# Kernel tuning notes

Hardware: AMD Instinct MI355X
Metric: run time of the kernel (lower is better)

## Reference

```python
import jax, jax.numpy as jnp
import numpy as np
import math

B, S, IN_DIM = 4, 2048, 512
D, H, L, FF = 256, 4, 4, 2048
HD = D // H
EPS = 1e-5


def _pos_encoding(S, D, dtype=jnp.float32):
    pos = jnp.arange(S, dtype=jnp.float32)[:, None]
    div = jnp.exp(jnp.arange(0, D, 2, dtype=jnp.float32) * (-math.log(10000.0) / D))
    pe = jnp.zeros((S, D), dtype=jnp.float32)
    pe = pe.at[:, 0::2].set(jnp.sin(pos * div))
    pe = pe.at[:, 1::2].set(jnp.cos(pos * div))
    return pe.astype(dtype)


def _layernorm(x, w, b):
    mu = jnp.mean(x, axis=-1, keepdims=True)
    var = jnp.var(x, axis=-1, keepdims=True)
    return (x - mu) * jax.lax.rsqrt(var + EPS) * w + b


def setup_inputs() -> dict:
    key = jax.random.key(0)
    ks = jax.random.split(key, 12)
    sc = 0.02
    inp = {
        "x": jax.random.normal(ks[0], (B, S, IN_DIM), dtype=jnp.float32),
        "W_in": jax.random.normal(ks[1], (D, IN_DIM), dtype=jnp.float32) * sc,
        "b_in": jnp.zeros((D,), dtype=jnp.float32),
        "qkv_w": jax.random.normal(ks[2], (L, 3 * D, D), dtype=jnp.float32) * sc,
        "qkv_b": jnp.zeros((L, 3 * D), dtype=jnp.float32),
        "out_w": jax.random.normal(ks[3], (L, D, D), dtype=jnp.float32) * sc,
        "out_b": jnp.zeros((L, D), dtype=jnp.float32),
        "ln1_w": jnp.ones((L, D), dtype=jnp.float32),
        "ln1_b": jnp.zeros((L, D), dtype=jnp.float32),
        "ff1_w": jax.random.normal(ks[4], (L, FF, D), dtype=jnp.float32) * sc,
        "ff1_b": jnp.zeros((L, FF), dtype=jnp.float32),
        "ff2_w": jax.random.normal(ks[5], (L, D, FF), dtype=jnp.float32) * sc,
        "ff2_b": jnp.zeros((L, D), dtype=jnp.float32),
        "ln2_w": jnp.ones((L, D), dtype=jnp.float32),
        "ln2_b": jnp.zeros((L, D), dtype=jnp.float32),
        "W_fc": jax.random.normal(ks[6], (IN_DIM, D), dtype=jnp.float32) * sc,
        "b_fc": jnp.zeros((IN_DIM,), dtype=jnp.float32),
    }
    return inp


def reference(x, W_in, b_in, qkv_w, qkv_b, out_w, out_b, ln1_w, ln1_b,
              ff1_w, ff1_b, ff2_w, ff2_b, ln2_w, ln2_b, W_fc, b_fc):
    # input projection + positional encoding (dropout=0 / eval)
    h = jnp.einsum('bsi,di->bsd', x, W_in) + b_in
    h = h + _pos_encoding(S, D, h.dtype)[None]

    scale = 1.0 / math.sqrt(HD)
    for l in range(L):
        # --- self-attention (unfused: explicit QK^T + softmax + V) ---
        qkv = jnp.einsum('bsd,ed->bse', h, qkv_w[l]) + qkv_b[l]  # [B,S,3D]
        q, k, v = jnp.split(qkv, 3, axis=-1)
        q = q.reshape(B, S, H, HD).transpose(0, 2, 1, 3)  # [B,H,S,HD]
        k = k.reshape(B, S, H, HD).transpose(0, 2, 1, 3)
        v = v.reshape(B, S, H, HD).transpose(0, 2, 1, 3)
        scores = jnp.einsum('bhqd,bhkd->bhqk', q, k) * scale  # [B,H,S,S]
        attn = jax.nn.softmax(scores, axis=-1)
        ctx = jnp.einsum('bhqk,bhkd->bhqd', attn, v)
        ctx = ctx.transpose(0, 2, 1, 3).reshape(B, S, D)
        sa = jnp.einsum('bsd,ed->bse', ctx, out_w[l]) + out_b[l]
        h = _layernorm(h + sa, ln1_w[l], ln1_b[l])  # post-norm
        # --- feed-forward (relu) ---
        ff = jax.nn.relu(jnp.einsum('bsd,fd->bsf', h, ff1_w[l]) + ff1_b[l])
        ff = jnp.einsum('bsf,df->bsd', ff, ff2_w[l]) + ff2_b[l]
        h = _layernorm(h + ff, ln2_w[l], ln2_b[l])

    # final projection from last time step
    return jnp.einsum('bd,od->bo', h[:, -1, :], W_fc) + b_fc  # [B, IN_DIM]
```

## Files before the change

kernel.cpp:

```cpp
#include <hip/hip_runtime.h>
#include <math.h>

#define S_LEN 2048
#define DMODEL 256
#define NHEAD 4
#define HDIM 64
#define NLAYER 4
#define FFDIM 2048
#define INDIM 512
#define BATCH 4
#define NTOK (BATCH * S_LEN)
#define EPSV 1e-5f
#define KSPLIT 4

typedef __attribute__((ext_vector_type(8))) short frag8;
typedef __attribute__((ext_vector_type(4))) float f32x4v;
typedef unsigned short u16;
typedef unsigned int u32;

__device__ __forceinline__ float pe_val(int s, int d) {
    const float c = 0.035977892f;
    float dv = expf(-(float)(d & ~1) * c);
    float arg = (float)s * dv;
    return (d & 1) ? cosf(arg) : sinf(arg);
}

__device__ __forceinline__ u16 f2bf(float f) {
    union { float f; unsigned u; } v; v.f = f;
    unsigned r = v.u + 0x7fffu + ((v.u >> 16) & 1u);
    return (u16)(r >> 16);
}
__device__ __forceinline__ float bf2f(u16 h) {
    union { u32 u; float f; } v; v.u = (u32)h << 16; return v.f;
}
__device__ __forceinline__ u32 pk2bf(float lo, float hi) {
    union { float f; u32 u; } a, b; a.f = lo; b.f = hi;
    return __builtin_amdgcn_perm(b.u, a.u, 0x07060302u);
}
__device__ __forceinline__ void load_lds16(const u16* g, u16* l) {
    __builtin_amdgcn_global_load_lds(
        (const __attribute__((address_space(1))) unsigned int*)g,
        (__attribute__((address_space(3))) unsigned int*)l, 16, 0, 0);
}

__global__ __launch_bounds__(256) void cvt_all(
    const float* __restrict__ x, const float* __restrict__ W_in,
    const float* __restrict__ qkv_w, const float* __restrict__ out_w,
    const float* __restrict__ ff1_w, const float* __restrict__ ff2_w,
    u16* __restrict__ xb, u16* __restrict__ W_in_b,
    u16* __restrict__ qkv_w_b, u16* __restrict__ out_w_b,
    u16* __restrict__ ff1_w_b, u16* __restrict__ ff2_w_b)
{
    const int i = blockIdx.x * 256 + threadIdx.x;
    const float* src; u16* dst; int base;
    if (i < 1048576)      { src = x;     dst = xb;      base = 0; }
    else if (i < 1081344) { src = W_in;  dst = W_in_b;  base = 1048576; }
    else if (i < 1277952) { src = qkv_w; dst = qkv_w_b; base = 1081344; }
    else if (i < 1343488) { src = out_w; dst = out_w_b; base = 1277952; }
    else if (i < 1867776) { src = ff1_w; dst = ff1_w_b; base = 1343488; }
    else                  { src = ff2_w; dst = ff2_w_b; base = 1867776; }
    const int e = (i - base) * 4;
    const float4 v = *(const float4*)(src + e);
    ushort4 o;
    o.x = f2bf(v.x); o.y = f2bf(v.y); o.z = f2bf(v.z); o.w = f2bf(v.w);
    *(ushort4*)(dst + e) = o;
}

template <int MODE>
__global__ __launch_bounds__(256) void gemm_mfma(
    const u16* __restrict__ A, const u16* __restrict__ W,
    const float* __restrict__ bias, u16* __restrict__ Cb,
    int M, int N, int K)
{
    __shared__ __align__(16) u16 As[128 * 32];
    __shared__ __align__(16) u16 Bs[128 * 32];
    const int t = threadIdx.x;
    const int w = t >> 6, lane = t & 63;
    const int col = lane & 15, quad = lane >> 4;
    const int qx = (quad ^ ((col >> 1) & 3)) * 8;
    const int m0 = blockIdx.x * 128, n0 = blockIdx.y * 128;
    const int wm = (w >> 1) * 64, wn = (w & 1) * 64;

    const int r0 = lane >> 2;
    const int kc = ((lane & 3) ^ ((lane >> 3) & 3)) * 8;
    const u16* pA0 = A + (size_t)(m0 + (w * 2 + 0) * 16 + r0) * K + kc;
    const u16* pA1 = A + (size_t)(m0 + (w * 2 + 1) * 16 + r0) * K + kc;
    const u16* pB0 = W + (size_t)(n0 + (w * 2 + 0) * 16 + r0) * K + kc;
    const u16* pB1 = W + (size_t)(n0 + (w * 2 + 1) * 16 + r0) * K + kc;
    u16* lA0 = As + (w * 2 + 0) * 512;
    u16* lA1 = As + (w * 2 + 1) * 512;
    u16* lB0 = Bs + (w * 2 + 0) * 512;
    u16* lB1 = Bs + (w * 2 + 1) * 512;

    f32x4v acc[4][4];
#pragma unroll
    for (int i = 0; i < 4; ++i)
#pragma unroll
        for (int j = 0; j < 4; ++j) acc[i][j] = (f32x4v){0.f, 0.f, 0.f, 0.f};

    for (int kb = 0; kb < K; kb += 32) {
        __syncthreads();
        load_lds16(pA0 + kb, lA0);
        load_lds16(pA1 + kb, lA1);
        load_lds16(pB0 + kb, lB0);
        load_lds16(pB1 + kb, lB1);
        __syncthreads();

        frag8 a[4], b[4];
#pragma unroll
        for (int i = 0; i < 4; ++i)
            a[i] = *(const frag8*)&As[(wm + i * 16 + col) * 32 + qx];
#pragma unroll
        for (int j = 0; j < 4; ++j)
            b[j] = *(const frag8*)&Bs[(wn + j * 16 + col) * 32 + qx];
#pragma unroll
        for (int i = 0; i < 4; ++i)
#pragma unroll
            for (int j = 0; j < 4; ++j)
                acc[i][j] = __builtin_amdgcn_mfma_f32_16x16x32_bf16(
                    a[i], b[j], acc[i][j], 0, 0, 0);
    }

#pragma unroll
    for (int j = 0; j < 4; ++j) {
        const int cn = n0 + wn + j * 16 + col;
        const float bv = bias[cn];
#pragma unroll
        for (int i = 0; i < 4; ++i) {
            const int cmb = m0 + wm + i * 16 + quad * 4;
#pragma unroll
            for (int r = 0; r < 4; ++r) {
                float v = acc[i][j][r] + bv;
                if (MODE == 2) v = fmaxf(v, 0.f);
                Cb[(size_t)(cmb + r) * N + cn] = f2bf(v);
            }
        }
    }
}

template <int MODE>
__global__ __launch_bounds__(256) void gemm64k(
    const u16* __restrict__ A, const u16* __restrict__ W,
    const float* __restrict__ bias, u16* __restrict__ Cb,
    u16* __restrict__ aux, const float* __restrict__ lp,
    int M, int N, int K)
{
    __shared__ __align__(16) u16 As[2][64 * 64];
    __shared__ __align__(16) u16 Bs[2][64 * 64];
    const int t = threadIdx.x;
    const int w = t >> 6, lane = t & 63;
    const int col = lane & 15, quad = lane >> 4;
    const int px0 = ((quad ^ (col & 7))) * 8;
    const int px1 = px0 ^ 32;
    const int m0 = blockIdx.x * 64, n0 = blockIdx.y * 64;
    const int wm = (w >> 1) * 32, wn = (w & 1) * 32;

    const int sr = lane >> 3;
    const int lc = ((lane & 7) ^ sr) * 8;
    const u16* pA0 = A + (size_t)(m0 + w * 16 + sr) * K + lc;
    const u16* pA1 = A + (size_t)(m0 + w * 16 + 8 + sr) * K + lc;
    const u16* pB0 = W + (size_t)(n0 + w * 16 + sr) * K + lc;
    const u16* pB1 = W + (size_t)(n0 + w * 16 + 8 + sr) * K + lc;
    const int o0 = (w * 16) * 64, o1 = (w * 16 + 8) * 64;

    f32x4v acc[2][2];
#pragma unroll
    for (int i = 0; i < 2; ++i)
#pragma unroll
        for (int j = 0; j < 2; ++j) acc[i][j] = (f32x4v){0.f, 0.f, 0.f, 0.f};

    auto stageA = [&](int it, int buf) {
        if (MODE == 6) {
            const int hh = it;
#pragma unroll
            for (int pos = 0; pos < 2; ++pos) {
                const int m = m0 + w * 16 + pos * 8 + sr;
                const int q = m & (S_LEN - 1);
                const int bh = (m >> 11) * 4 + hh;
                const size_t basei = (((size_t)bh) * S_LEN + q) * 64 + lc;
                float l = 0.f;
                float o[8] = {0.f, 0.f, 0.f, 0.f, 0.f, 0.f, 0.f, 0.f};
#pragma unroll
                for (int ksx = 0; ksx < KSPLIT; ++ksx) {
                    const uint4 pv = *(const uint4*)(A + (size_t)ksx * 16 * S_LEN * 64 + basei);
                    o[0] += bf2f((u16)(pv.x & 0xffff)); o[1] += bf2f((u16)(pv.x >> 16));
                    o[2] += bf2f((u16)(pv.y & 0xffff)); o[3] += bf2f((u16)(pv.y >> 16));
                    o[4] += bf2f((u16)(pv.z & 0xffff)); o[5] += bf2f((u16)(pv.z >> 16));
                    o[6] += bf2f((u16)(pv.w & 0xffff)); o[7] += bf2f((u16)(pv.w >> 16));
                    l += lp[((size_t)ksx * 16 + bh) * S_LEN + q];
                }
                const float inv = 1.f / l;
                uint4 pk;
                pk.x = ((u32)f2bf(o[1] * inv) << 16) | f2bf(o[0] * inv);
                pk.y = ((u32)f2bf(o[3] * inv) << 16) | f2bf(o[2] * inv);
                pk.z = ((u32)f2bf(o[5] * inv) << 16) | f2bf(o[4] * inv);
                pk.w = ((u32)f2bf(o[7] * inv) << 16) | f2bf(o[6] * inv);
                *(uint4*)&As[buf][(pos ? o1 : o0) + lane * 8] = pk;
            }
        } else {
            const int kb = it << 6;
            load_lds16(pA0 + kb, &As[buf][o0]);
            load_lds16(pA1 + kb, &As[buf][o1]);
        }
    };
    auto stageB = [&](int it, int buf) {
        const int kb = it << 6;
        load_lds16(pB0 + kb, &Bs[buf][o0]);
        load_lds16(pB1 + kb, &Bs[buf][o1]);
    };

    stageA(0, 0);
    stageB(0, 0);

    const int NIT = K >> 6;
    for (int it = 0; it < NIT; ++it) {
        const int cur = it & 1;
        __syncthreads();
        if (it + 1 < NIT) {
            stageA(it + 1, cur ^ 1);
            stageB(it + 1, cur ^ 1);
        }
#pragma unroll
        for (int kh = 0; kh < 2; ++kh) {
            const int px = kh ? px1 : px0;
            frag8 a[2], b[2];
#pragma unroll
            for (int i = 0; i < 2; ++i)
                a[i] = *(const frag8*)&As[cur][(wm + i * 16 + col) * 64 + px];
#pragma unroll
            for (int j = 0; j < 2; ++j)
                b[j] = *(const frag8*)&Bs[cur][(wn + j * 16 + col) * 64 + px];
#pragma unroll
            for (int i = 0; i < 2; ++i)
#pragma unroll
                for (int j = 0; j < 2; ++j)
                    acc[i][j] = __builtin_amdgcn_mfma_f32_16x16x32_bf16(
                        a[i], b[j], acc[i][j], 0, 0, 0);
        }
    }

#pragma unroll
    for (int j = 0; j < 2; ++j) {
        const int cn = n0 + wn + j * 16 + col;
        const float bv = bias[cn];
#pragma unroll
        for (int i = 0; i < 2; ++i) {
            const int cmb = m0 + wm + i * 16 + quad * 4;
            float vv[4];
#pragma unroll
            for (int r = 0; r < 4; ++r) {
                float v = acc[i][j][r] + bv;
                if (MODE == 1) v += pe_val((cmb + r) & (S_LEN - 1), cn);
                if (MODE == 5 || MODE == 6)
                    v += bf2f(aux[(size_t)(cmb + r) * N + cn]);
                vv[r] = v;
                Cb[(size_t)(cmb + r) * N + cn] = f2bf(v);
            }
            if (MODE == 4 && cn >= 512) {
                const int dg = cn - 512;
                const int bh = (cmb >> 11) * 4 + (dg >> 6);
                uint2 pk;
                pk.x = ((u32)f2bf(vv[1]) << 16) | f2bf(vv[0]);
                pk.y = ((u32)f2bf(vv[3]) << 16) | f2bf(vv[2]);
                *(uint2*)&aux[((size_t)bh * 64 + (dg & 63)) * S_LEN + (cmb & 2047)] = pk;
            }
        }
    }
}

__global__ __launch_bounds__(256) void attn_part(const u16* __restrict__ qkv,
                                                 const u16* __restrict__ vt,
                                                 u16* __restrict__ Opart,
                                                 float* __restrict__ lpart)
{
    __shared__ __align__(16) u16 Ks0[64 * 32], Ks1[64 * 32];
    __shared__ __align__(16) u16 Vt0[64 * 32], Vt1[64 * 32];
    __shared__ __align__(16) u16 Ps[4][2][2][512];

    const int t = threadIdx.x;
    const int w = t >> 6, lane = t & 63;
    const int col = lane & 15, quad = lane >> 4;
    const int sq = (col >> 1) & 3;
    const int qx = (quad ^ sq) * 8;
    const int bh = blockIdx.x, b = bh >> 2, hh = bh & 3;
    const int qt = blockIdx.y, ks = blockIdx.z;

    const float SCL = 0.125f * 1.44269504f;

    frag8 qf[2][2];
#pragma unroll
    for (int qg = 0; qg < 2; ++qg) {
        const int qrow = qt * 128 + w * 32 + qg * 16 + col;
        const u16* qp = qkv + (size_t)(b * S_LEN + qrow) * 768 + hh * HDIM;
        const frag8 r0 = *(const frag8*)(qp + quad * 8);
        const frag8 r1 = *(const frag8*)(qp + 32 + quad * 8);
#pragma unroll
        for (int e = 0; e < 8; ++e) {
            qf[qg][0][e] = (short)f2bf(bf2f((u16)r0[e]) * SCL);
            qf[qg][1][e] = (short)f2bf(bf2f((u16)r1[e]) * SCL);
        }
    }
    frag8 ones;
#pragma unroll
    for (int e = 0; e < 8; ++e) ones[e] = (short)0x3F80;

    f32x4v Oacc[2][4], lacc[2];
#pragma unroll
    for (int qg = 0; qg < 2; ++qg) {
#pragma unroll
        for (int dt = 0; dt < 4; ++dt) Oacc[qg][dt] = (f32x4v){0.f, 0.f, 0.f, 0.f};
        lacc[qg] = (f32x4v){0.f, 0.f, 0.f, 0.f};
    }

    const int srow = w * 16 + (lane >> 2);
    const int sseg = ((lane & 3) ^ ((lane >> 3) & 3)) * 8;
    const int kb0 = ks * (S_LEN / KSPLIT);
    const u16* kbase = qkv + (size_t)(b * S_LEN + kb0 + srow) * 768
                       + 256 + hh * HDIM + sseg;
    const u16* vbase = vt + ((size_t)bh * 64 + srow) * S_LEN + kb0 + sseg;
    u16* lK0 = Ks0 + w * 512;
    u16* lK1 = Ks1 + w * 512;
    u16* lV0 = Vt0 + w * 512;
    u16* lV1 = Vt1 + w * 512;

    for (int kt = 0; kt < S_LEN / KSPLIT / 64; ++kt) {
        __syncthreads();
        const u16* kp = kbase + (size_t)kt * 64 * 768;
        const u16* vp = vbase + kt * 64;
        load_lds16(kp, lK0);
        load_lds16(kp + 32, lK1);
        load_lds16(vp, lV0);
        load_lds16(vp + 32, lV1);
        __syncthreads();

#pragma unroll
        for (int nt = 0; nt < 4; ++nt) {
            const frag8 k0 = *(const frag8*)&Ks0[(nt * 16 + col) * 32 + qx];
            const frag8 k1 = *(const frag8*)&Ks1[(nt * 16 + col) * 32 + qx];
            const int c = (nt & 1) * 2 + (quad >> 1);
            const int poff = col * 32 + ((c ^ sq) * 8) + (quad & 1) * 4;
#pragma unroll
            for (int qg = 0; qg < 2; ++qg) {
                f32x4v s = (f32x4v){0.f, 0.f, 0.f, 0.f};
                s = __builtin_amdgcn_mfma_f32_16x16x32_bf16(k0, qf[qg][0], s, 0, 0, 0);
                s = __builtin_amdgcn_mfma_f32_16x16x32_bf16(k1, qf[qg][1], s, 0, 0, 0);
                const float p0 = __builtin_amdgcn_exp2f(s[0]);
                const float p1 = __builtin_amdgcn_exp2f(s[1]);
                const float p2 = __builtin_amdgcn_exp2f(s[2]);
                const float p3 = __builtin_amdgcn_exp2f(s[3]);
                uint2 pk;
                pk.x = pk2bf(p0, p1);
                pk.y = pk2bf(p2, p3);
                *(uint2*)&Ps[w][qg][nt >> 1][poff] = pk;
            }
        }

        frag8 pf[2][2];
#pragma unroll
        for (int qg = 0; qg < 2; ++qg) {
            pf[qg][0] = *(const frag8*)&Ps[w][qg][0][col * 32 + qx];
            pf[qg][1] = *(const frag8*)&Ps[w][qg][1][col * 32 + qx];
        }
#pragma unroll
        for (int dt = 0; dt < 4; ++dt) {
            const frag8 v0 = *(const frag8*)&Vt0[(dt * 16 + col) * 32 + qx];
            const frag8 v1 = *(const frag8*)&Vt1[(dt * 16 + col) * 32 + qx];
#pragma unroll
            for (int qg = 0; qg < 2; ++qg) {
                Oacc[qg][dt] = __builtin_amdgcn_mfma_f32_16x16x32_bf16(
                    v0, pf[qg][0], Oacc[qg][dt], 0, 0, 0);
                Oacc[qg][dt] = __builtin_amdgcn_mfma_f32_16x16x32_bf16(
                    v1, pf[qg][1], Oacc[qg][dt], 0, 0, 0);
            }
        }
#pragma unroll
        for (int qg = 0; qg < 2; ++qg) {
            lacc[qg] = __builtin_amdgcn_mfma_f32_16x16x32_bf16(
                ones, pf[qg][0], lacc[qg], 0, 0, 0);
            lacc[qg] = __builtin_amdgcn_mfma_f32_16x16x32_bf16(
                ones, pf[qg][1], lacc[qg], 0, 0, 0);
        }
    }

#pragma unroll
    for (int qg = 0; qg < 2; ++qg) {
        const int qrow = qt * 128 + w * 32 + qg * 16 + col;
        u16* op = Opart + (((size_t)ks * 16 + bh) * S_LEN + qrow) * 64;
#pragma unroll
        for (int dt = 0; dt < 4; ++dt) {
            uint2 pk;
            pk.x = pk2bf(Oacc[qg][dt][0], Oacc[qg][dt][1]);
            pk.y = pk2bf(Oacc[qg][dt][2], Oacc[qg][dt][3]);
            *(uint2*)(op + dt * 16 + quad * 4) = pk;
        }
        if (quad == 0)
            lpart[((size_t)ks * 16 + bh) * S_LEN + qrow] = lacc[qg][0];
    }
}

__global__ __launch_bounds__(256) void ln_only(u16* __restrict__ hb,
                                               const u16* __restrict__ sab,
                                               const float* __restrict__ w,
                                               const float* __restrict__ b)
{
    const int t = blockIdx.x;
    const int d = threadIdx.x;
    const size_t idx = (size_t)t * DMODEL + d;
    const float x = bf2f(sab[idx]);

    float s = x, s2 = x * x;
#pragma unroll
    for (int off = 32; off; off >>= 1) {
        s += __shfl_down(s, off);
        s2 += __shfl_down(s2, off);
    }
    __shared__ float ls[4], ls2[4];
    __shared__ float mu_s, rs_s;
    const int wid = d >> 6, lane = d & 63;
    if (lane == 0) { ls[wid] = s; ls2[wid] = s2; }
    __syncthreads();
    if (d == 0) {
        const float ts = ls[0] + ls[1] + ls[2] + ls[3];
        const float ts2 = ls2[0] + ls2[1] + ls2[2] + ls2[3];
        const float mu = ts * (1.f / DMODEL);
        const float var = ts2 * (1.f / DMODEL) - mu * mu;
        mu_s = mu;
        rs_s = rsqrtf(var + EPSV);
    }
    __syncthreads();
    hb[idx] = f2bf((x - mu_s) * rs_s * w[d] + b[d]);
}

__global__ __launch_bounds__(256) void final_proj(const u16* __restrict__ hb,
                                                  const float* __restrict__ Wfc,
                                                  const float* __restrict__ bfc,
                                                  float* __restrict__ out)
{
    const int idx = blockIdx.x * 256 + threadIdx.x;
    const int b = idx >> 9;
    const int o = idx & 511;
    const u16* hp = hb + (size_t)(b * S_LEN + S_LEN - 1) * DMODEL;
    const float* wp = Wfc + (size_t)o * DMODEL;
    float s = 0.f;
#pragma unroll 4
    for (int d = 0; d < DMODEL; ++d) s += bf2f(hp[d]) * wp[d];
    out[idx] = s + bfc[o];
}

extern "C" void kernel_launch(void* const* d_in, const int* in_sizes, int n_in,
                              void* d_out, int out_size, void* d_ws, size_t ws_size,
                              hipStream_t stream)
{
    const float* x     = (const float*)d_in[0];
    const float* W_in  = (const float*)d_in[1];
    const float* b_in  = (const float*)d_in[2];
    const float* qkv_w = (const float*)d_in[3];
    const float* qkv_b = (const float*)d_in[4];
    const float* out_w = (const float*)d_in[5];
    const float* out_b = (const float*)d_in[6];
    const float* ln1_w = (const float*)d_in[7];
    const float* ln1_b = (const float*)d_in[8];
    const float* ff1_w = (const float*)d_in[9];
    const float* ff1_b = (const float*)d_in[10];
    const float* ff2_w = (const float*)d_in[11];
    const float* ff2_b = (const float*)d_in[12];
    const float* ln2_w = (const float*)d_in[13];
    const float* ln2_b = (const float*)d_in[14];
    const float* W_fc  = (const float*)d_in[15];
    const float* b_fc  = (const float*)d_in[16];
    float* out = (float*)d_out;

    char* p = (char*)d_ws;
    u16* hb    = (u16*)p;  p += (size_t)NTOK * DMODEL * 2;
    u16* sab   = (u16*)p;  p += (size_t)NTOK * DMODEL * 2;
    u16* xb    = (u16*)p;  p += (size_t)NTOK * INDIM * 2;
    u16* qkvb  = (u16*)p;  p += (size_t)NTOK * 768 * 2;
    u16* ffb   = (u16*)p;  p += (size_t)NTOK * FFDIM * 2;
    u16* vtb   = (u16*)p;  p += (size_t)16 * 64 * S_LEN * 2;
    float* lpart = (float*)p; p += (size_t)KSPLIT * 16 * S_LEN * 4;
    u16* W_in_b  = (u16*)p; p += (size_t)131072 * 2;
    u16* qkv_w_b = (u16*)p; p += (size_t)786432 * 2;
    u16* out_w_b = (u16*)p; p += (size_t)262144 * 2;
    u16* ff1_w_b = (u16*)p; p += (size_t)2097152 * 2;
    u16* ff2_w_b = (u16*)p; p += (size_t)2097152 * 2;
    if (ws_size < (size_t)78643200) return;

    u16* Opart = ffb;

    cvt_all<<<9344, 256, 0, stream>>>(x, W_in, qkv_w, out_w, ff1_w, ff2_w,
                                      xb, W_in_b, qkv_w_b, out_w_b, ff1_w_b, ff2_w_b);

    gemm64k<1><<<dim3(NTOK / 64, DMODEL / 64), 256, 0, stream>>>(
        xb, W_in_b, b_in, hb, nullptr, nullptr, NTOK, DMODEL, INDIM);

    for (int l = 0; l < NLAYER; ++l) {
        gemm64k<4><<<dim3(NTOK / 64, 768 / 64), 256, 0, stream>>>(
            hb, qkv_w_b + (size_t)l * 768 * DMODEL, qkv_b + l * 768,
            qkvb, vtb, nullptr, NTOK, 768, DMODEL);
        attn_part<<<dim3(BATCH * NHEAD, S_LEN / 128, KSPLIT), 256, 0, stream>>>(
            qkvb, vtb, Opart, lpart);
        gemm64k<6><<<dim3(NTOK / 64, DMODEL / 64), 256, 0, stream>>>(
            Opart, out_w_b + (size_t)l * DMODEL * DMODEL, out_b + l * DMODEL,
            sab, hb, lpart, NTOK, DMODEL, DMODEL);
        ln_only<<<NTOK, 256, 0, stream>>>(hb, sab, ln1_w + l * DMODEL, ln1_b + l * DMODEL);
        gemm_mfma<2><<<dim3(NTOK / 128, FFDIM / 128), 256, 0, stream>>>(
            hb, ff1_w_b + (size_t)l * FFDIM * DMODEL, ff1_b + l * FFDIM,
            ffb, NTOK, FFDIM, DMODEL);
        gemm64k<5><<<dim3(NTOK / 64, DMODEL / 64), 256, 0, stream>>>(
            ffb, ff2_w_b + (size_t)l * DMODEL * FFDIM, ff2_b + l * DMODEL,
            sab, hb, nullptr, NTOK, DMODEL, FFDIM);
        ln_only<<<NTOK, 256, 0, stream>>>(hb, sab, ln2_w + l * DMODEL, ln2_b + l * DMODEL);
    }

    final_proj<<<8, 256, 0, stream>>>(hb, W_fc, b_fc, out);
}
```

Measured before the change: 552.6 us.

## Double-buffer LDS in GEMM and attention, use one-wave-per-row layernorm

The MFMA GEMM and the attention kernel now keep two LDS buffers and prefetch the next K tile while computing on the current one, which removes one barrier per iteration. The attention kernel also interleaves the QK/exp/P-write per query group so the P buffer is halved. Layernorm is rewritten so each wave handles one row with vectorized loads and xor shuffles, dropping the block-level reductions and barriers. Double buffering raises LDS usage, which may lower occupancy. With a single barrier per iteration, the reuse of the shared P buffer across query groups within a wave relies on wave-level ordering.

```diff
diff --git a/kernel.cpp b/kernel.cpp
--- a/kernel.cpp
+++ b/kernel.cpp
@@ -72,8 +72,8 @@
     const float* __restrict__ bias, u16* __restrict__ Cb,
     int M, int N, int K)
 {
-    __shared__ __align__(16) u16 As[128 * 32];
-    __shared__ __align__(16) u16 Bs[128 * 32];
+    __shared__ __align__(16) u16 As[2][128 * 32];
+    __shared__ __align__(16) u16 Bs[2][128 * 32];
     const int t = threadIdx.x;
     const int w = t >> 6, lane = t & 63;
     const int col = lane & 15, quad = lane >> 4;
@@ -87,10 +87,7 @@
     const u16* pA1 = A + (size_t)(m0 + (w * 2 + 1) * 16 + r0) * K + kc;
     const u16* pB0 = W + (size_t)(n0 + (w * 2 + 0) * 16 + r0) * K + kc;
     const u16* pB1 = W + (size_t)(n0 + (w * 2 + 1) * 16 + r0) * K + kc;
-    u16* lA0 = As + (w * 2 + 0) * 512;
-    u16* lA1 = As + (w * 2 + 1) * 512;
-    u16* lB0 = Bs + (w * 2 + 0) * 512;
-    u16* lB1 = Bs + (w * 2 + 1) * 512;
+    const int oA0 = (w * 2 + 0) * 512, oA1 = (w * 2 + 1) * 512;
 
     f32x4v acc[4][4];
 #pragma unroll
@@ -98,21 +95,30 @@
 #pragma unroll
         for (int j = 0; j < 4; ++j) acc[i][j] = (f32x4v){0.f, 0.f, 0.f, 0.f};
 
-    for (int kb = 0; kb < K; kb += 32) {
+    load_lds16(pA0, &As[0][oA0]);
+    load_lds16(pA1, &As[0][oA1]);
+    load_lds16(pB0, &Bs[0][oA0]);
+    load_lds16(pB1, &Bs[0][oA1]);
+
+    const int NIT = K >> 5;
+    for (int it = 0; it < NIT; ++it) {
+        const int cur = it & 1;
         __syncthreads();
-        load_lds16(pA0 + kb, lA0);
-        load_lds16(pA1 + kb, lA1);
-        load_lds16(pB0 + kb, lB0);
-        load_lds16(pB1 + kb, lB1);
-        __syncthreads();
+        if (it + 1 < NIT) {
+            const int kb = (it + 1) << 5;
+            load_lds16(pA0 + kb, &As[cur ^ 1][oA0]);
+            load_lds16(pA1 + kb, &As[cur ^ 1][oA1]);
+            load_lds16(pB0 + kb, &Bs[cur ^ 1][oA0]);
+            load_lds16(pB1 + kb, &Bs[cur ^ 1][oA1]);
+        }
 
         frag8 a[4], b[4];
 #pragma unroll
         for (int i = 0; i < 4; ++i)
-            a[i] = *(const frag8*)&As[(wm + i * 16 + col) * 32 + qx];
+            a[i] = *(const frag8*)&As[cur][(wm + i * 16 + col) * 32 + qx];
 #pragma unroll
         for (int j = 0; j < 4; ++j)
-            b[j] = *(const frag8*)&Bs[(wn + j * 16 + col) * 32 + qx];
+            b[j] = *(const frag8*)&Bs[cur][(wn + j * 16 + col) * 32 + qx];
 #pragma unroll
         for (int i = 0; i < 4; ++i)
 #pragma unroll
@@ -273,9 +279,9 @@
                                                  u16* __restrict__ Opart,
                                                  float* __restrict__ lpart)
 {
-    __shared__ __align__(16) u16 Ks0[64 * 32], Ks1[64 * 32];
-    __shared__ __align__(16) u16 Vt0[64 * 32], Vt1[64 * 32];
-    __shared__ __align__(16) u16 Ps[4][2][2][512];
+    __shared__ __align__(16) u16 Ks[2][2][64 * 32];
+    __shared__ __align__(16) u16 Vt[2][2][64 * 32];
+    __shared__ __align__(16) u16 Ps[4][2][512];
 
     const int t = threadIdx.x;
     const int w = t >> 6, lane = t & 63;
@@ -318,29 +324,33 @@
     const u16* kbase = qkv + (size_t)(b * S_LEN + kb0 + srow) * 768
                        + 256 + hh * HDIM + sseg;
     const u16* vbase = vt + ((size_t)bh * 64 + srow) * S_LEN + kb0 + sseg;
-    u16* lK0 = Ks0 + w * 512;
-    u16* lK1 = Ks1 + w * 512;
-    u16* lV0 = Vt0 + w * 512;
-    u16* lV1 = Vt1 + w * 512;
-
-    for (int kt = 0; kt < S_LEN / KSPLIT / 64; ++kt) {
+    const int so = w * 512;
+
+    load_lds16(kbase, &Ks[0][0][so]);
+    load_lds16(kbase + 32, &Ks[0][1][so]);
+    load_lds16(vbase, &Vt[0][0][so]);
+    load_lds16(vbase + 32, &Vt[0][1][so]);
+
+    const int NT = S_LEN / KSPLIT / 64;
+    for (int kt = 0; kt < NT; ++kt) {
+        const int cur = kt & 1;
         __syncthreads();
-        const u16* kp = kbase + (size_t)kt * 64 * 768;
-        const u16* vp = vbase + kt * 64;
-        load_lds16(kp, lK0);
-        load_lds16(kp + 32, lK1);
-        load_lds16(vp, lV0);
-        load_lds16(vp + 32, lV1);
-        __syncthreads();
-
-#pragma unroll
-        for (int nt = 0; nt < 4; ++nt) {
-            const frag8 k0 = *(const frag8*)&Ks0[(nt * 16 + col) * 32 + qx];
-            const frag8 k1 = *(const frag8*)&Ks1[(nt * 16 + col) * 32 + qx];
-            const int c = (nt & 1) * 2 + (quad >> 1);
-            const int poff = col * 32 + ((c ^ sq) * 8) + (quad & 1) * 4;
-#pragma unroll
-            for (int qg = 0; qg < 2; ++qg) {
+        if (kt + 1 < NT) {
+            const u16* kp = kbase + (size_t)(kt + 1) * 64 * 768;
+            const u16* vp = vbase + (kt + 1) * 64;
+            load_lds16(kp, &Ks[cur ^ 1][0][so]);
+            load_lds16(kp + 32, &Ks[cur ^ 1][1][so]);
+            load_lds16(vp, &Vt[cur ^ 1][0][so]);
+            load_lds16(vp + 32, &Vt[cur ^ 1][1][so]);
+        }
+
+        frag8 pf[2][2];
+#pragma unroll
+        for (int qg = 0; qg < 2; ++qg) {
+#pragma unroll
+            for (int nt = 0; nt < 4; ++nt) {
+                const frag8 k0 = *(const frag8*)&Ks[cur][0][(nt * 16 + col) * 32 + qx];
+                const frag8 k1 = *(const frag8*)&Ks[cur][1][(nt * 16 + col) * 32 + qx];
                 f32x4v s = (f32x4v){0.f, 0.f, 0.f, 0.f};
                 s = __builtin_amdgcn_mfma_f32_16x16x32_bf16(k0, qf[qg][0], s, 0, 0, 0);
                 s = __builtin_amdgcn_mfma_f32_16x16x32_bf16(k1, qf[qg][1], s, 0, 0, 0);
@@ -348,23 +358,21 @@
                 const float p1 = __builtin_amdgcn_exp2f(s[1]);
                 const float p2 = __builtin_amdgcn_exp2f(s[2]);
                 const float p3 = __builtin_amdgcn_exp2f(s[3]);
+                const int c = (nt & 1) * 2 + (quad >> 1);
+                const int poff = col * 32 + ((c ^ sq) * 8) + (quad & 1) * 4;
                 uint2 pk;
                 pk.x = pk2bf(p0, p1);
                 pk.y = pk2bf(p2, p3);
-                *(uint2*)&Ps[w][qg][nt >> 1][poff] = pk;
+                *(uint2*)&Ps[w][nt >> 1][poff] = pk;
             }
-        }
-
-        frag8 pf[2][2];
-#pragma unroll
-        for (int qg = 0; qg < 2; ++qg) {
-            pf[qg][0] = *(const frag8*)&Ps[w][qg][0][col * 32 + qx];
-            pf[qg][1] = *(const frag8*)&Ps[w][qg][1][col * 32 + qx];
-        }
+            pf[qg][0] = *(const frag8*)&Ps[w][0][col * 32 + qx];
+            pf[qg][1] = *(const frag8*)&Ps[w][1][col * 32 + qx];
+        }
+
 #pragma unroll
         for (int dt = 0; dt < 4; ++dt) {
-            const frag8 v0 = *(const frag8*)&Vt0[(dt * 16 + col) * 32 + qx];
-            const frag8 v1 = *(const frag8*)&Vt1[(dt * 16 + col) * 32 + qx];
+            const frag8 v0 = *(const frag8*)&Vt[cur][0][(dt * 16 + col) * 32 + qx];
+            const frag8 v1 = *(const frag8*)&Vt[cur][1][(dt * 16 + col) * 32 + qx];
 #pragma unroll
             for (int qg = 0; qg < 2; ++qg) {
                 Oacc[qg][dt] = __builtin_amdgcn_mfma_f32_16x16x32_bf16(
@@ -398,37 +406,39 @@
     }
 }
 
-__global__ __launch_bounds__(256) void ln_only(u16* __restrict__ hb,
+__global__ __launch_bounds__(256) void ln_wave(u16* __restrict__ hb,
                                                const u16* __restrict__ sab,
                                                const float* __restrict__ w,
                                                const float* __restrict__ b)
 {
-    const int t = blockIdx.x;
-    const int d = threadIdx.x;
-    const size_t idx = (size_t)t * DMODEL + d;
-    const float x = bf2f(sab[idx]);
-
-    float s = x, s2 = x * x;
-#pragma unroll
-    for (int off = 32; off; off >>= 1) {
-        s += __shfl_down(s, off);
-        s2 += __shfl_down(s2, off);
-    }
-    __shared__ float ls[4], ls2[4];
-    __shared__ float mu_s, rs_s;
-    const int wid = d >> 6, lane = d & 63;
-    if (lane == 0) { ls[wid] = s; ls2[wid] = s2; }
-    __syncthreads();
-    if (d == 0) {
-        const float ts = ls[0] + ls[1] + ls[2] + ls[3];
-        const float ts2 = ls2[0] + ls2[1] + ls2[2] + ls2[3];
-        const float mu = ts * (1.f / DMODEL);
-        const float var = ts2 * (1.f / DMODEL) - mu * mu;
-        mu_s = mu;
-        rs_s = rsqrtf(var + EPSV);
-    }
-    __syncthreads();
-    hb[idx] = f2bf((x - mu_s) * rs_s * w[d] + b[d]);
+    const int t = threadIdx.x;
+    const int wv = t >> 6, lane = t & 63;
+    const int row = blockIdx.x * 4 + wv;
+    const size_t base = (size_t)row * DMODEL + lane * 4;
+
+    const ushort4 xv = *(const ushort4*)&sab[base];
+    const float x0 = bf2f(xv.x), x1 = bf2f(xv.y);
+    const float x2 = bf2f(xv.z), x3 = bf2f(xv.w);
+
+    float s = (x0 + x1) + (x2 + x3);
+    float s2 = (x0 * x0 + x1 * x1) + (x2 * x2 + x3 * x3);
+#pragma unroll
+    for (int msk = 1; msk < 64; msk <<= 1) {
+        s += __shfl_xor(s, msk);
+        s2 += __shfl_xor(s2, msk);
+    }
+    const float mu = s * (1.f / DMODEL);
+    const float var = s2 * (1.f / DMODEL) - mu * mu;
+    const float rs = rsqrtf(var + EPSV);
+
+    const float4 wv4 = *(const float4*)&w[lane * 4];
+    const float4 bv4 = *(const float4*)&b[lane * 4];
+    ushort4 o;
+    o.x = f2bf((x0 - mu) * rs * wv4.x + bv4.x);
+    o.y = f2bf((x1 - mu) * rs * wv4.y + bv4.y);
+    o.z = f2bf((x2 - mu) * rs * wv4.z + bv4.z);
+    o.w = f2bf((x3 - mu) * rs * wv4.w + bv4.w);
+    *(ushort4*)&hb[base] = o;
 }
 
 __global__ __launch_bounds__(256) void final_proj(const u16* __restrict__ hb,
@@ -502,14 +512,14 @@
         gemm64k<6><<<dim3(NTOK / 64, DMODEL / 64), 256, 0, stream>>>(
             Opart, out_w_b + (size_t)l * DMODEL * DMODEL, out_b + l * DMODEL,
             sab, hb, lpart, NTOK, DMODEL, DMODEL);
-        ln_only<<<NTOK, 256, 0, stream>>>(hb, sab, ln1_w + l * DMODEL, ln1_b + l * DMODEL);
+        ln_wave<<<NTOK / 4, 256, 0, stream>>>(hb, sab, ln1_w + l * DMODEL, ln1_b + l * DMODEL);
         gemm_mfma<2><<<dim3(NTOK / 128, FFDIM / 128), 256, 0, stream>>>(
             hb, ff1_w_b + (size_t)l * FFDIM * DMODEL, ff1_b + l * FFDIM,
             ffb, NTOK, FFDIM, DMODEL);
         gemm64k<5><<<dim3(NTOK / 64, DMODEL / 64), 256, 0, stream>>>(
             ffb, ff2_w_b + (size_t)l * DMODEL * FFDIM, ff2_b + l * DMODEL,
             sab, hb, nullptr, NTOK, DMODEL, FFDIM);
-        ln_only<<<NTOK, 256, 0, stream>>>(hb, sab, ln2_w + l * DMODEL, ln2_b + l * DMODEL);
+        ln_wave<<<NTOK / 4, 256, 0, stream>>>(hb, sab, ln2_w + l * DMODEL, ln2_b + l * DMODEL);
     }
 
     final_proj<<<8, 256, 0, stream>>>(hb, W_fc, b_fc, out);
```

Result: faster. 534.9 us (-3.2%).
